# Performance work log

Measured on AMD Instinct MI355X. Metric: run time of the kernel, lower is better.

Reference implementation:

```python
import jax, jax.numpy as jnp
import numpy as np

NUM_USERS = 4096
NUM_ITEMS = 8192
EMBED_DIM = 64
NUM_LAYERS = 3


def setup_inputs() -> dict:
    key = jax.random.key(0)
    k1, k2 = jax.random.split(key)
    # embedding table for users+items (nn.Embedding init normal std=0.1)
    x = jax.random.normal(k1, (NUM_USERS + NUM_ITEMS, EMBED_DIM), dtype=jnp.float32) * 0.1
    # dense 0/1 user-item interaction matrix (forward applies torch.nonzero to it)
    edge_index = jax.random.randint(k2, (NUM_USERS, NUM_ITEMS), 0, 2, dtype=jnp.int32)
    return {"x": x, "edge_index": edge_index}


def reference(x, edge_index):
    U, I, L = NUM_USERS, NUM_ITEMS, NUM_LAYERS
    adj = edge_index.astype(jnp.float32)  # [U, I], 0/1
    # symmetric degree normalization: adj / sqrt(deg_u * deg_i), nan (0/0) -> 0
    deg_u = jnp.sum(adj, axis=1)  # [U]
    deg_i = jnp.sum(adj, axis=0)  # [I]
    denom = jnp.sqrt(deg_u[:, None] * deg_i[None, :])  # [U, I]
    weights = jnp.where(denom > 0, adj / jnp.where(denom > 0, denom, 1.0), 0.0)
    # weights is identical every layer (depends only on edge_index)
    acc = jnp.zeros_like(x)
    for _ in range(L):
        # NOTE: original code concatenates (item-side, user-side) in this order
        x = jnp.concatenate([weights.T @ x[:U], weights @ x[U:]], axis=0)  # [I+U, d]
        acc = acc + x
    # alpha = 1/(1+L) * ones applied to every layer output
    return acc / (1.0 + L)
```

## Files before the change

### kernel.cpp

```cpp
#include <hip/hip_runtime.h>

#define NU 4096
#define NI 8192
#define ND 64
#define NTOT 12288
#define CT 8
#define CB 16
#define BROW 520

typedef unsigned short u16;
typedef unsigned int u32;
typedef unsigned long long u64;

__device__ __forceinline__ u16 f2bf(float f) {
    union { float f; u32 u; } v; v.f = f;
    u32 u = v.u;
    u += 0x7FFFu + ((u >> 16) & 1u);
    return (u16)(u >> 16);
}

typedef short frag8 __attribute__((ext_vector_type(8)));
typedef float f32x4 __attribute__((ext_vector_type(4)));

__global__ __launch_bounds__(256) void k_pack2(const int* __restrict__ edge,
        u64* __restrict__ Apk, u64* __restrict__ ATpk) {
    __shared__ __align__(16) u16 At[256][40];
    __shared__ __align__(16) u64 Tt[512][6];
    const int t = threadIdx.x;
    const int u0 = (blockIdx.x >> 4) * 256;
    const int i0 = (blockIdx.x & 15) * 512;
    const int cg = t & 31;
    const int rb = t >> 5;

    #pragma unroll 4
    for (int rr = 0; rr < 32; rr++) {
        const int row = rb * 32 + rr;
        const int4* p = (const int4*)(edge + (size_t)(u0 + row) * NI + i0 + cg * 16);
        u32 bits = 0;
        #pragma unroll
        for (int m = 0; m < 4; m++) {
            int4 v = p[m];
            bits |= (v.x != 0 ? 1u : 0u) << (m * 4 + 0);
            bits |= (v.y != 0 ? 1u : 0u) << (m * 4 + 1);
            bits |= (v.z != 0 ? 1u : 0u) << (m * 4 + 2);
            bits |= (v.w != 0 ? 1u : 0u) << (m * 4 + 3);
        }
        At[row][cg] = (u16)bits;
    }
    __syncthreads();

    {
        u64* dst = Apk + (size_t)(u0 + t) * 128 + (i0 >> 6);
        #pragma unroll
        for (int q = 0; q < 4; q++) {
            uint4 v = *(const uint4*)&At[t][q * 8];
            *(uint4*)(dst + q * 2) = v;
        }
    }

    {
        const int lane = t & 63, w = t >> 6;
        const u64 M[6] = {0x00000000FFFFFFFFULL, 0x0000FFFF0000FFFFULL,
                          0x00FF00FF00FF00FFULL, 0x0F0F0F0F0F0F0F0FULL,
                          0x3333333333333333ULL, 0x5555555555555555ULL};
        #pragma unroll
        for (int sc = 0; sc < 8; sc++) {
            u64 x = *(const u64*)&At[w * 64 + lane][sc * 4];
            #pragma unroll
            for (int si = 0; si < 6; si++) {
                const int s = 32 >> si;
                u64 y = __shfl_xor(x, s, 64);
                x = (lane & s) ? ((x & ~M[si]) | ((y >> s) & M[si]))
                               : ((x &  M[si]) | ((y << s) & ~M[si]));
            }
            Tt[sc * 64 + lane][w] = x;
        }
    }
    __syncthreads();
    #pragma unroll
    for (int j = 0; j < 2; j++) {
        const int item = t * 2 + j;
        ulonglong2 a = *(const ulonglong2*)&Tt[item][0];
        ulonglong2 b = *(const ulonglong2*)&Tt[item][2];
        u64* dst = ATpk + (size_t)(i0 + item) * 64 + (u0 >> 6);
        *(ulonglong2*)dst = a;
        *(ulonglong2*)(dst + 2) = b;
    }
}

__global__ __launch_bounds__(256) void k_scale0(const float* __restrict__ x,
        const u64* __restrict__ Apk, const u64* __restrict__ ATpk,
        float* __restrict__ dsu, float* __restrict__ dsi,
        u16* __restrict__ BuT, u16* __restrict__ BiT) {
    __shared__ float sc[64];
    const int t = threadIdx.x;
    const int r0 = blockIdx.x * 64;
    {
        const int rl = t >> 2, part = t & 3;
        int cnt = 0;
        if (r0 < NU) {
            const u64* p = Apk + (size_t)(r0 + rl) * 128 + part * 32;
            #pragma unroll
            for (int i = 0; i < 32; i++) cnt += (int)__popcll(p[i]);
        } else {
            const u64* p = ATpk + (size_t)(r0 - NU + rl) * 64 + part * 16;
            #pragma unroll
            for (int i = 0; i < 16; i++) cnt += (int)__popcll(p[i]);
        }
        cnt += __shfl_xor(cnt, 1, 64);
        cnt += __shfl_xor(cnt, 2, 64);
        if (part == 0) {
            float s = cnt > 0 ? rsqrtf((float)cnt) : 0.f;
            sc[rl] = s;
            if (r0 < NU) dsu[r0 + rl] = s; else dsi[r0 - NU + rl] = s;
        }
    }
    __syncthreads();
    const int r4 = t >> 4, c4 = t & 15;
    float y[4][4];
    #pragma unroll
    for (int j = 0; j < 4; j++) {
        const int rl = r4 * 4 + j;
        const float s = sc[rl];
        float4 xv = *(const float4*)(x + (size_t)(r0 + rl) * ND + c4 * 4);
        y[j][0] = xv.x * s; y[j][1] = xv.y * s;
        y[j][2] = xv.z * s; y[j][3] = xv.w * s;
    }
    u16* dst; size_t stride; int col0;
    if (r0 < NU) { dst = BuT; stride = NU; col0 = r0; }
    else         { dst = BiT; stride = NI; col0 = r0 - NU; }
    #pragma unroll
    for (int k = 0; k < 4; k++) {
        ushort4 w;
        w.x = f2bf(y[0][k]); w.y = f2bf(y[1][k]);
        w.z = f2bf(y[2][k]); w.w = f2bf(y[3][k]);
        *(ushort4*)(dst + (size_t)(c4 * 4 + k) * stride + col0 + r4 * 4) = w;
    }
}

__global__ __launch_bounds__(256) void k_gemm(
        const u64* __restrict__ Apk, const u64* __restrict__ ATpk,
        const u16* __restrict__ BuT, const u16* __restrict__ BiT,
        float* __restrict__ Ptop, float* __restrict__ Pbot) {
    __shared__ __align__(16) u16 Bs[64 * BROW];
    const int t = threadIdx.x, bx = blockIdx.x;
    const int lane = t & 63, w = t >> 6, lr = lane & 15, lg = lane >> 4;
    const u64* arow; const u16* dense; int Kstr, wpr, kbase, pstr; float* Pout;
    if (bx < 1024) {
        const int tile = bx >> 3, chunk = bx & 7;
        arow = ATpk + (size_t)(tile * 64) * 64 + chunk * 8; wpr = 64;
        dense = BuT; Kstr = NU; kbase = chunk * 512; pstr = CT * 64;
        Pout = Ptop + (size_t)(tile * 64) * pstr + chunk * 64;
    } else {
        const int b2 = bx - 1024, tile = b2 >> 4, chunk = b2 & 15;
        arow = Apk + (size_t)(tile * 64) * 128 + chunk * 8; wpr = 128;
        dense = BiT; Kstr = NI; kbase = chunk * 512; pstr = CB * 64;
        Pout = Pbot + (size_t)(tile * 64) * pstr + chunk * 64;
    }
    const u16* gsrc = dense + kbase;
    #pragma unroll
    for (int it = 0; it < 16; it++) {
        const int e = it * 4 + w;
        __builtin_amdgcn_global_load_lds(
            (const __attribute__((address_space(1))) void*)
                (gsrc + (size_t)e * Kstr + lane * 8),
            (__attribute__((address_space(3))) void*)(&Bs[e * BROW]),
            16, 0, 0);
    }
    const u64* myrow = arow + (size_t)(w * 16 + lr) * wpr;
    u64 aw[8];
    #pragma unroll
    for (int qq = 0; qq < 4; qq++) {
        ulonglong2 v = *(const ulonglong2*)(myrow + qq * 2);
        aw[qq * 2] = v.x; aw[qq * 2 + 1] = v.y;
    }
    f32x4 acc[4];
    #pragma unroll
    for (int i = 0; i < 4; i++) acc[i] = f32x4{0.f, 0.f, 0.f, 0.f};
    __syncthreads();

    #pragma unroll
    for (int kk = 0; kk < 8; kk++) {
        const u32 lo = (u32)aw[kk], hi = (u32)(aw[kk] >> 32);
        const u32 byte0 = (lo >> (lg * 8)) & 0xFFu;
        const u32 byte1 = (hi >> (lg * 8)) & 0xFFu;
        frag8 bf0, bf1;
        #pragma unroll
        for (int j = 0; j < 8; j++) {
            bf0[j] = (short)(((byte0 >> j) & 1u) ? 0x3F80 : 0);
            bf1[j] = (short)(((byte1 >> j) & 1u) ? 0x3F80 : 0);
        }
        #pragma unroll
        for (int nt = 0; nt < 4; nt++) {
            const int e = nt * 16 + lr;
            frag8 a0 = *(const frag8*)&Bs[e * BROW + kk * 64 + lg * 8];
            frag8 a1 = *(const frag8*)&Bs[e * BROW + kk * 64 + 32 + lg * 8];
            acc[nt] = __builtin_amdgcn_mfma_f32_16x16x32_bf16(a0, bf0, acc[nt], 0, 0, 0);
            acc[nt] = __builtin_amdgcn_mfma_f32_16x16x32_bf16(a1, bf1, acc[nt], 0, 0, 0);
        }
    }
    __syncthreads();
    float* Fs = (float*)Bs;
    #pragma unroll
    for (int nt = 0; nt < 4; nt++) {
        const int row = w * 16 + lr, g = nt * 4 + lg;
        *(f32x4*)&Fs[row * 64 + (((g + row) & 15) * 4)] = acc[nt];
    }
    __syncthreads();
    #pragma unroll
    for (int ii = 0; ii < 4; ii++) {
        const int slot = t + ii * 256;
        const int row = slot >> 4, g = slot & 15;
        f32x4 v = *(const f32x4*)&Fs[row * 64 + (((g + row) & 15) * 4)];
        *(f32x4*)&Pout[(size_t)row * pstr + g * 4] = v;
    }
}

__global__ __launch_bounds__(256) void k_reduce(
        const float* __restrict__ Ptop, const float* __restrict__ Pbot,
        const float* __restrict__ dsu, const float* __restrict__ dsi,
        float* __restrict__ accbuf, u16* __restrict__ BuTn,
        u16* __restrict__ BiTn, float* __restrict__ out, int layer) {
    __shared__ u16 TB[64][24];
    const int t = threadIdx.x, bx = blockIdx.x;
    const int rl = t >> 4, e4 = t & 15;
    int grow; float so;
    float sx = 0.f, sy = 0.f, sz = 0.f, sw = 0.f;
    if (bx < 512) {
        grow = bx * 16 + rl;
        const float* p = Ptop + (size_t)grow * (CT * 64) + e4 * 4;
        #pragma unroll
        for (int c = 0; c < CT; c++) {
            float4 v = *(const float4*)(p + c * 64);
            sx += v.x; sy += v.y; sz += v.z; sw += v.w;
        }
        so = dsi[grow];
    } else {
        const int u = (bx - 512) * 16 + rl;
        grow = NI + u;
        const float* p = Pbot + (size_t)u * (CB * 64) + e4 * 4;
        #pragma unroll
        for (int c = 0; c < CB; c++) {
            float4 v = *(const float4*)(p + c * 64);
            sx += v.x; sy += v.y; sz += v.z; sw += v.w;
        }
        so = dsu[grow - NI];
    }
    float4 y;
    y.x = sx * so; y.y = sy * so; y.z = sz * so; y.w = sw * so;
    const size_t o = (size_t)grow * ND + e4 * 4;
    if (layer == 0) {
        *(float4*)(accbuf + o) = y;
    } else if (layer == 1) {
        float4 a = *(const float4*)(accbuf + o);
        a.x += y.x; a.y += y.y; a.z += y.z; a.w += y.w;
        *(float4*)(accbuf + o) = a;
    } else {
        float4 a = *(const float4*)(accbuf + o);
        a.x = (a.x + y.x) * 0.25f; a.y = (a.y + y.y) * 0.25f;
        a.z = (a.z + y.z) * 0.25f; a.w = (a.w + y.w) * 0.25f;
        *(float4*)(out + o) = a;
    }
    if (layer != 2) {
        const float fn = (grow < NU) ? dsu[grow] : dsi[grow - NU];
        TB[e4 * 4 + 0][rl] = f2bf(y.x * fn);
        TB[e4 * 4 + 1][rl] = f2bf(y.y * fn);
        TB[e4 * 4 + 2][rl] = f2bf(y.z * fn);
        TB[e4 * 4 + 3][rl] = f2bf(y.w * fn);
        __syncthreads();
        if (t < 128) {
            const int e = t >> 1, h = t & 1;
            u16* dst; size_t stride; int col0;
            if (bx < 256)      { dst = BuTn; stride = NU; col0 = bx * 16; }
            else if (bx < 512) { dst = BiTn; stride = NI; col0 = bx * 16 - NU; }
            else               { dst = BiTn; stride = NI; col0 = (bx - 512) * 16 + NI - NU; }
            uint4 v = *(const uint4*)&TB[e][h * 8];
            *(uint4*)(dst + (size_t)e * stride + col0 + h * 8) = v;
        }
    }
}

extern "C" void kernel_launch(void* const* d_in, const int* in_sizes, int n_in,
                              void* d_out, int out_size, void* d_ws, size_t ws_size,
                              hipStream_t stream) {
    (void)in_sizes; (void)n_in; (void)out_size; (void)ws_size;
    const float* x    = (const float*)d_in[0];
    const int*   edge = (const int*)d_in[1];
    float* out = (float*)d_out;

    char* ws = (char*)d_ws;
    size_t off = 0;
    u64* Apk  = (u64*)(ws + off); off += (size_t)NU * (NI / 64) * 8;
    u64* ATpk = (u64*)(ws + off); off += (size_t)NI * (NU / 64) * 8;
    float* dsu = (float*)(ws + off); off += (size_t)NU * 4;
    float* dsi = (float*)(ws + off); off += (size_t)NI * 4;
    u16* BuT0 = (u16*)(ws + off); off += (size_t)ND * NU * 2;
    u16* BuT1 = (u16*)(ws + off); off += (size_t)ND * NU * 2;
    u16* BiT0 = (u16*)(ws + off); off += (size_t)ND * NI * 2;
    u16* BiT1 = (u16*)(ws + off); off += (size_t)ND * NI * 2;
    float* acc  = (float*)(ws + off); off += (size_t)NTOT * ND * 4;
    float* Ptop = (float*)(ws + off); off += (size_t)NI * CT * 64 * 4;
    float* Pbot = (float*)(ws + off); off += (size_t)NU * CB * 64 * 4;

    k_pack2<<<256, 256, 0, stream>>>(edge, Apk, ATpk);
    k_scale0<<<NTOT / 64, 256, 0, stream>>>(x, Apk, ATpk, dsu, dsi, BuT0, BiT0);

    k_gemm<<<2048, 256, 0, stream>>>(Apk, ATpk, BuT0, BiT0, Ptop, Pbot);
    k_reduce<<<768, 256, 0, stream>>>(Ptop, Pbot, dsu, dsi, acc, BuT1, BiT1, out, 0);
    k_gemm<<<2048, 256, 0, stream>>>(Apk, ATpk, BuT1, BiT1, Ptop, Pbot);
    k_reduce<<<768, 256, 0, stream>>>(Ptop, Pbot, dsu, dsi, acc, BuT0, BiT0, out, 1);
    k_gemm<<<2048, 256, 0, stream>>>(Apk, ATpk, BuT0, BiT0, Ptop, Pbot);
    k_reduce<<<768, 256, 0, stream>>>(Ptop, Pbot, dsu, dsi, acc,
                                      (u16*)nullptr, (u16*)nullptr, out, 2);
}
```

Before: 287.9 us.

## Fuse split-K reduction into GEMM via last-block atomic counter; shrink pack tiles

```diff
diff --git a/kernel.cpp b/kernel.cpp
--- a/kernel.cpp
+++ b/kernel.cpp
@@ -7,6 +7,7 @@
 #define CT 8
 #define CB 16
 #define BROW 520
+#define NTILE 192
 
 typedef unsigned short u16;
 typedef unsigned int u32;
@@ -24,17 +25,17 @@
 
 __global__ __launch_bounds__(256) void k_pack2(const int* __restrict__ edge,
         u64* __restrict__ Apk, u64* __restrict__ ATpk) {
-    __shared__ __align__(16) u16 At[256][40];
-    __shared__ __align__(16) u64 Tt[512][6];
+    __shared__ __align__(16) u16 At[128][40];
+    __shared__ __align__(16) u64 Tt[512][2];
     const int t = threadIdx.x;
-    const int u0 = (blockIdx.x >> 4) * 256;
+    const int u0 = (blockIdx.x >> 4) * 128;
     const int i0 = (blockIdx.x & 15) * 512;
     const int cg = t & 31;
     const int rb = t >> 5;
 
     #pragma unroll 4
-    for (int rr = 0; rr < 32; rr++) {
-        const int row = rb * 32 + rr;
+    for (int rr = 0; rr < 16; rr++) {
+        const int row = rb * 16 + rr;
         const int4* p = (const int4*)(edge + (size_t)(u0 + row) * NI + i0 + cg * 16);
         u32 bits = 0;
         #pragma unroll
@@ -50,12 +51,12 @@
     __syncthreads();
 
     {
-        u64* dst = Apk + (size_t)(u0 + t) * 128 + (i0 >> 6);
-        #pragma unroll
-        for (int q = 0; q < 4; q++) {
-            uint4 v = *(const uint4*)&At[t][q * 8];
-            *(uint4*)(dst + q * 2) = v;
-        }
+        const int row = t >> 1, h = t & 1;
+        uint4 v0 = *(const uint4*)&At[row][h * 16];
+        uint4 v1 = *(const uint4*)&At[row][h * 16 + 8];
+        u64* dst = Apk + (size_t)(u0 + row) * 128 + (i0 >> 6) + h * 4;
+        *(uint4*)dst = v0;
+        *(uint4*)(dst + 2) = v1;
     }
 
     {
@@ -64,8 +65,10 @@
                           0x00FF00FF00FF00FFULL, 0x0F0F0F0F0F0F0F0FULL,
                           0x3333333333333333ULL, 0x5555555555555555ULL};
         #pragma unroll
-        for (int sc = 0; sc < 8; sc++) {
-            u64 x = *(const u64*)&At[w * 64 + lane][sc * 4];
+        for (int m = 0; m < 4; m++) {
+            const int id = m * 4 + w;
+            const int sr = id >> 3, sc = id & 7;
+            u64 x = *(const u64*)&At[sr * 64 + lane][sc * 4];
             #pragma unroll
             for (int si = 0; si < 6; si++) {
                 const int s = 32 >> si;
@@ -73,7 +76,7 @@
                 x = (lane & s) ? ((x & ~M[si]) | ((y >> s) & M[si]))
                                : ((x &  M[si]) | ((y << s) & ~M[si]));
             }
-            Tt[sc * 64 + lane][w] = x;
+            Tt[sc * 64 + lane][sr] = x;
         }
     }
     __syncthreads();
@@ -81,10 +84,7 @@
     for (int j = 0; j < 2; j++) {
         const int item = t * 2 + j;
         ulonglong2 a = *(const ulonglong2*)&Tt[item][0];
-        ulonglong2 b = *(const ulonglong2*)&Tt[item][2];
-        u64* dst = ATpk + (size_t)(i0 + item) * 64 + (u0 >> 6);
-        *(ulonglong2*)dst = a;
-        *(ulonglong2*)(dst + 2) = b;
+        *(ulonglong2*)(ATpk + (size_t)(i0 + item) * 64 + (u0 >> 6)) = a;
     }
 }
 
@@ -138,24 +138,32 @@
     }
 }
 
-__global__ __launch_bounds__(256) void k_gemm(
+__global__ __launch_bounds__(256) void k_gemmf(
         const u64* __restrict__ Apk, const u64* __restrict__ ATpk,
         const u16* __restrict__ BuT, const u16* __restrict__ BiT,
-        float* __restrict__ Ptop, float* __restrict__ Pbot) {
+        float* __restrict__ Ptop, float* __restrict__ Pbot,
+        const float* __restrict__ dsu, const float* __restrict__ dsi,
+        float* __restrict__ accbuf, u16* __restrict__ BuTn,
+        u16* __restrict__ BiTn, float* __restrict__ out,
+        int* __restrict__ cnt, int layer) {
     __shared__ __align__(16) u16 Bs[64 * BROW];
+    __shared__ int isLast;
     const int t = threadIdx.x, bx = blockIdx.x;
     const int lane = t & 63, w = t >> 6, lr = lane & 15, lg = lane >> 4;
-    const u64* arow; const u16* dense; int Kstr, wpr, kbase, pstr; float* Pout;
+    const u64* arow; const u16* dense; int Kstr, wpr, kbase, pstr, tile, tileId, nch;
+    float* Pout; bool top;
     if (bx < 1024) {
-        const int tile = bx >> 3, chunk = bx & 7;
+        tile = bx >> 3; const int chunk = bx & 7; top = true;
         arow = ATpk + (size_t)(tile * 64) * 64 + chunk * 8; wpr = 64;
         dense = BuT; Kstr = NU; kbase = chunk * 512; pstr = CT * 64;
         Pout = Ptop + (size_t)(tile * 64) * pstr + chunk * 64;
+        tileId = tile; nch = CT;
     } else {
-        const int b2 = bx - 1024, tile = b2 >> 4, chunk = b2 & 15;
+        const int b2 = bx - 1024; tile = b2 >> 4; const int chunk = b2 & 15; top = false;
         arow = Apk + (size_t)(tile * 64) * 128 + chunk * 8; wpr = 128;
         dense = BiT; Kstr = NI; kbase = chunk * 512; pstr = CB * 64;
         Pout = Pbot + (size_t)(tile * 64) * pstr + chunk * 64;
+        tileId = 128 + tile; nch = CB;
     }
     const u16* gsrc = dense + kbase;
     #pragma unroll
@@ -214,69 +222,86 @@
         f32x4 v = *(const f32x4*)&Fs[row * 64 + (((g + row) & 15) * 4)];
         *(f32x4*)&Pout[(size_t)row * pstr + g * 4] = v;
     }
-}
-
-__global__ __launch_bounds__(256) void k_reduce(
-        const float* __restrict__ Ptop, const float* __restrict__ Pbot,
-        const float* __restrict__ dsu, const float* __restrict__ dsi,
-        float* __restrict__ accbuf, u16* __restrict__ BuTn,
-        u16* __restrict__ BiTn, float* __restrict__ out, int layer) {
-    __shared__ u16 TB[64][24];
-    const int t = threadIdx.x, bx = blockIdx.x;
-    const int rl = t >> 4, e4 = t & 15;
+    __syncthreads();
+    if (t == 0) {
+        __builtin_amdgcn_fence(__ATOMIC_RELEASE, "agent");
+        int old = __hip_atomic_fetch_add(&cnt[tileId], 1,
+                                         __ATOMIC_RELAXED, __HIP_MEMORY_SCOPE_AGENT);
+        isLast = (old == nch - 1);
+    }
+    __syncthreads();
+    if (!isLast) return;
+
+    __builtin_amdgcn_fence(__ATOMIC_ACQUIRE, "agent");
+    const int r = t >> 2, q = t & 3;
     int grow; float so;
-    float sx = 0.f, sy = 0.f, sz = 0.f, sw = 0.f;
-    if (bx < 512) {
-        grow = bx * 16 + rl;
-        const float* p = Ptop + (size_t)grow * (CT * 64) + e4 * 4;
+    float4 s0 = {0,0,0,0}, s1 = {0,0,0,0}, s2 = {0,0,0,0}, s3 = {0,0,0,0};
+    if (top) {
+        grow = tile * 64 + r;
+        const float* p = Ptop + (size_t)grow * (CT * 64) + q * 16;
         #pragma unroll
         for (int c = 0; c < CT; c++) {
-            float4 v = *(const float4*)(p + c * 64);
-            sx += v.x; sy += v.y; sz += v.z; sw += v.w;
+            s0.x += p[c*64+0];  s0.y += p[c*64+1];  s0.z += p[c*64+2];  s0.w += p[c*64+3];
+            s1.x += p[c*64+4];  s1.y += p[c*64+5];  s1.z += p[c*64+6];  s1.w += p[c*64+7];
+            s2.x += p[c*64+8];  s2.y += p[c*64+9];  s2.z += p[c*64+10]; s2.w += p[c*64+11];
+            s3.x += p[c*64+12]; s3.y += p[c*64+13]; s3.z += p[c*64+14]; s3.w += p[c*64+15];
         }
         so = dsi[grow];
     } else {
-        const int u = (bx - 512) * 16 + rl;
+        const int u = tile * 64 + r;
         grow = NI + u;
-        const float* p = Pbot + (size_t)u * (CB * 64) + e4 * 4;
+        const float* p = Pbot + (size_t)u * (CB * 64) + q * 16;
         #pragma unroll
         for (int c = 0; c < CB; c++) {
-            float4 v = *(const float4*)(p + c * 64);
-            sx += v.x; sy += v.y; sz += v.z; sw += v.w;
-        }
-        so = dsu[grow - NI];
-    }
-    float4 y;
-    y.x = sx * so; y.y = sy * so; y.z = sz * so; y.w = sw * so;
-    const size_t o = (size_t)grow * ND + e4 * 4;
-    if (layer == 0) {
-        *(float4*)(accbuf + o) = y;
-    } else if (layer == 1) {
-        float4 a = *(const float4*)(accbuf + o);
-        a.x += y.x; a.y += y.y; a.z += y.z; a.w += y.w;
-        *(float4*)(accbuf + o) = a;
-    } else {
-        float4 a = *(const float4*)(accbuf + o);
-        a.x = (a.x + y.x) * 0.25f; a.y = (a.y + y.y) * 0.25f;
-        a.z = (a.z + y.z) * 0.25f; a.w = (a.w + y.w) * 0.25f;
-        *(float4*)(out + o) = a;
+            s0.x += p[c*64+0];  s0.y += p[c*64+1];  s0.z += p[c*64+2];  s0.w += p[c*64+3];
+            s1.x += p[c*64+4];  s1.y += p[c*64+5];  s1.z += p[c*64+6];  s1.w += p[c*64+7];
+            s2.x += p[c*64+8];  s2.y += p[c*64+9];  s2.z += p[c*64+10]; s2.w += p[c*64+11];
+            s3.x += p[c*64+12]; s3.y += p[c*64+13]; s3.z += p[c*64+14]; s3.w += p[c*64+15];
+        }
+        so = dsu[u];
+    }
+    float4 y[4];
+    y[0].x = s0.x*so; y[0].y = s0.y*so; y[0].z = s0.z*so; y[0].w = s0.w*so;
+    y[1].x = s1.x*so; y[1].y = s1.y*so; y[1].z = s1.z*so; y[1].w = s1.w*so;
+    y[2].x = s2.x*so; y[2].y = s2.y*so; y[2].z = s2.z*so; y[2].w = s2.w*so;
+    y[3].x = s3.x*so; y[3].y = s3.y*so; y[3].z = s3.z*so; y[3].w = s3.w*so;
+    #pragma unroll
+    for (int j = 0; j < 4; j++) {
+        const size_t o = (size_t)grow * ND + q * 16 + j * 4;
+        if (layer == 0) {
+            *(float4*)(accbuf + o) = y[j];
+        } else if (layer == 1) {
+            float4 a = *(const float4*)(accbuf + o);
+            a.x += y[j].x; a.y += y[j].y; a.z += y[j].z; a.w += y[j].w;
+            *(float4*)(accbuf + o) = a;
+        } else {
+            float4 a = *(const float4*)(accbuf + o);
+            a.x = (a.x + y[j].x) * 0.25f; a.y = (a.y + y[j].y) * 0.25f;
+            a.z = (a.z + y[j].z) * 0.25f; a.w = (a.w + y[j].w) * 0.25f;
+            *(float4*)(out + o) = a;
+        }
     }
     if (layer != 2) {
         const float fn = (grow < NU) ? dsu[grow] : dsi[grow - NU];
-        TB[e4 * 4 + 0][rl] = f2bf(y.x * fn);
-        TB[e4 * 4 + 1][rl] = f2bf(y.y * fn);
-        TB[e4 * 4 + 2][rl] = f2bf(y.z * fn);
-        TB[e4 * 4 + 3][rl] = f2bf(y.w * fn);
+        u16* TB = (u16*)Bs;
+        #pragma unroll
+        for (int j = 0; j < 4; j++) {
+            TB[(q * 16 + j * 4 + 0) * 72 + r] = f2bf(y[j].x * fn);
+            TB[(q * 16 + j * 4 + 1) * 72 + r] = f2bf(y[j].y * fn);
+            TB[(q * 16 + j * 4 + 2) * 72 + r] = f2bf(y[j].z * fn);
+            TB[(q * 16 + j * 4 + 3) * 72 + r] = f2bf(y[j].w * fn);
+        }
         __syncthreads();
-        if (t < 128) {
-            const int e = t >> 1, h = t & 1;
-            u16* dst; size_t stride; int col0;
-            if (bx < 256)      { dst = BuTn; stride = NU; col0 = bx * 16; }
-            else if (bx < 512) { dst = BiTn; stride = NI; col0 = bx * 16 - NU; }
-            else               { dst = BiTn; stride = NI; col0 = (bx - 512) * 16 + NI - NU; }
-            uint4 v = *(const uint4*)&TB[e][h * 8];
-            *(uint4*)(dst + (size_t)e * stride + col0 + h * 8) = v;
-        }
+        u16* dst; size_t stride; int col0;
+        if (top) {
+            if (tile < 64) { dst = BuTn; stride = NU; col0 = tile * 64; }
+            else           { dst = BiTn; stride = NI; col0 = tile * 64 - NU; }
+        } else             { dst = BiTn; stride = NI; col0 = (NI - NU) + tile * 64; }
+        const int n = t >> 2, part = t & 3;
+        uint4 a = *(const uint4*)&TB[n * 72 + part * 16];
+        uint4 b = *(const uint4*)&TB[n * 72 + part * 16 + 8];
+        *(uint4*)(dst + (size_t)n * stride + col0 + part * 16) = a;
+        *(uint4*)(dst + (size_t)n * stride + col0 + part * 16 + 8) = b;
     }
 }
 
@@ -301,15 +326,17 @@
     float* acc  = (float*)(ws + off); off += (size_t)NTOT * ND * 4;
     float* Ptop = (float*)(ws + off); off += (size_t)NI * CT * 64 * 4;
     float* Pbot = (float*)(ws + off); off += (size_t)NU * CB * 64 * 4;
-
-    k_pack2<<<256, 256, 0, stream>>>(edge, Apk, ATpk);
+    int* cnt = (int*)(ws + off); off += (size_t)3 * NTILE * 4;
+
+    hipMemsetAsync(cnt, 0, 3 * NTILE * sizeof(int), stream);
+    k_pack2<<<512, 256, 0, stream>>>(edge, Apk, ATpk);
     k_scale0<<<NTOT / 64, 256, 0, stream>>>(x, Apk, ATpk, dsu, dsi, BuT0, BiT0);
 
-    k_gemm<<<2048, 256, 0, stream>>>(Apk, ATpk, BuT0, BiT0, Ptop, Pbot);
-    k_reduce<<<768, 256, 0, stream>>>(Ptop, Pbot, dsu, dsi, acc, BuT1, BiT1, out, 0);
-    k_gemm<<<2048, 256, 0, stream>>>(Apk, ATpk, BuT1, BiT1, Ptop, Pbot);
-    k_reduce<<<768, 256, 0, stream>>>(Ptop, Pbot, dsu, dsi, acc, BuT0, BiT0, out, 1);
-    k_gemm<<<2048, 256, 0, stream>>>(Apk, ATpk, BuT0, BiT0, Ptop, Pbot);
-    k_reduce<<<768, 256, 0, stream>>>(Ptop, Pbot, dsu, dsi, acc,
-                                      (u16*)nullptr, (u16*)nullptr, out, 2);
-}
+    k_gemmf<<<2048, 256, 0, stream>>>(Apk, ATpk, BuT0, BiT0, Ptop, Pbot,
+                                      dsu, dsi, acc, BuT1, BiT1, out, cnt, 0);
+    k_gemmf<<<2048, 256, 0, stream>>>(Apk, ATpk, BuT1, BiT1, Ptop, Pbot,
+                                      dsu, dsi, acc, BuT0, BiT0, out, cnt + NTILE, 1);
+    k_gemmf<<<2048, 256, 0, stream>>>(Apk, ATpk, BuT0, BiT0, Ptop, Pbot,
+                                      dsu, dsi, acc, (u16*)nullptr, (u16*)nullptr,
+                                      out, cnt + 2 * NTILE, 2);
+}
```

After: 695.6 us. 142% more time.

## Load GEMM dense operand directly from global and halve pack tile height

Applied to the files above, without the earlier changes.

```diff
diff --git a/kernel.cpp b/kernel.cpp
--- a/kernel.cpp
+++ b/kernel.cpp
@@ -6,7 +6,6 @@
 #define NTOT 12288
 #define CT 8
 #define CB 16
-#define BROW 520
 
 typedef unsigned short u16;
 typedef unsigned int u32;
@@ -24,17 +23,17 @@
 
 __global__ __launch_bounds__(256) void k_pack2(const int* __restrict__ edge,
         u64* __restrict__ Apk, u64* __restrict__ ATpk) {
-    __shared__ __align__(16) u16 At[256][40];
-    __shared__ __align__(16) u64 Tt[512][6];
+    __shared__ __align__(16) u16 At[128][40];
+    __shared__ __align__(16) u64 Tt[512][2];
     const int t = threadIdx.x;
-    const int u0 = (blockIdx.x >> 4) * 256;
+    const int u0 = (blockIdx.x >> 4) * 128;
     const int i0 = (blockIdx.x & 15) * 512;
     const int cg = t & 31;
     const int rb = t >> 5;
 
     #pragma unroll 4
-    for (int rr = 0; rr < 32; rr++) {
-        const int row = rb * 32 + rr;
+    for (int rr = 0; rr < 16; rr++) {
+        const int row = rb * 16 + rr;
         const int4* p = (const int4*)(edge + (size_t)(u0 + row) * NI + i0 + cg * 16);
         u32 bits = 0;
         #pragma unroll
@@ -50,12 +49,12 @@
     __syncthreads();
 
     {
-        u64* dst = Apk + (size_t)(u0 + t) * 128 + (i0 >> 6);
-        #pragma unroll
-        for (int q = 0; q < 4; q++) {
-            uint4 v = *(const uint4*)&At[t][q * 8];
-            *(uint4*)(dst + q * 2) = v;
-        }
+        const int row = t >> 1, h = t & 1;
+        uint4 v0 = *(const uint4*)&At[row][h * 16];
+        uint4 v1 = *(const uint4*)&At[row][h * 16 + 8];
+        u64* dst = Apk + (size_t)(u0 + row) * 128 + (i0 >> 6) + h * 4;
+        *(uint4*)dst = v0;
+        *(uint4*)(dst + 2) = v1;
     }
 
     {
@@ -64,8 +63,10 @@
                           0x00FF00FF00FF00FFULL, 0x0F0F0F0F0F0F0F0FULL,
                           0x3333333333333333ULL, 0x5555555555555555ULL};
         #pragma unroll
-        for (int sc = 0; sc < 8; sc++) {
-            u64 x = *(const u64*)&At[w * 64 + lane][sc * 4];
+        for (int m = 0; m < 4; m++) {
+            const int id = m * 4 + w;
+            const int sr = id >> 3, sc = id & 7;
+            u64 x = *(const u64*)&At[sr * 64 + lane][sc * 4];
             #pragma unroll
             for (int si = 0; si < 6; si++) {
                 const int s = 32 >> si;
@@ -73,7 +74,7 @@
                 x = (lane & s) ? ((x & ~M[si]) | ((y >> s) & M[si]))
                                : ((x &  M[si]) | ((y << s) & ~M[si]));
             }
-            Tt[sc * 64 + lane][w] = x;
+            Tt[sc * 64 + lane][sr] = x;
         }
     }
     __syncthreads();
@@ -81,10 +82,7 @@
     for (int j = 0; j < 2; j++) {
         const int item = t * 2 + j;
         ulonglong2 a = *(const ulonglong2*)&Tt[item][0];
-        ulonglong2 b = *(const ulonglong2*)&Tt[item][2];
-        u64* dst = ATpk + (size_t)(i0 + item) * 64 + (u0 >> 6);
-        *(ulonglong2*)dst = a;
-        *(ulonglong2*)(dst + 2) = b;
+        *(ulonglong2*)(ATpk + (size_t)(i0 + item) * 64 + (u0 >> 6)) = a;
     }
 }
 
@@ -142,7 +140,7 @@
         const u64* __restrict__ Apk, const u64* __restrict__ ATpk,
         const u16* __restrict__ BuT, const u16* __restrict__ BiT,
         float* __restrict__ Ptop, float* __restrict__ Pbot) {
-    __shared__ __align__(16) u16 Bs[64 * BROW];
+    __shared__ __align__(16) float Fs[64 * 64];
     const int t = threadIdx.x, bx = blockIdx.x;
     const int lane = t & 63, w = t >> 6, lr = lane & 15, lg = lane >> 4;
     const u64* arow; const u16* dense; int Kstr, wpr, kbase, pstr; float* Pout;
@@ -157,16 +155,6 @@
         dense = BiT; Kstr = NI; kbase = chunk * 512; pstr = CB * 64;
         Pout = Pbot + (size_t)(tile * 64) * pstr + chunk * 64;
     }
-    const u16* gsrc = dense + kbase;
-    #pragma unroll
-    for (int it = 0; it < 16; it++) {
-        const int e = it * 4 + w;
-        __builtin_amdgcn_global_load_lds(
-            (const __attribute__((address_space(1))) void*)
-                (gsrc + (size_t)e * Kstr + lane * 8),
-            (__attribute__((address_space(3))) void*)(&Bs[e * BROW]),
-            16, 0, 0);
-    }
     const u64* myrow = arow + (size_t)(w * 16 + lr) * wpr;
     u64 aw[8];
     #pragma unroll
@@ -174,10 +162,14 @@
         ulonglong2 v = *(const ulonglong2*)(myrow + qq * 2);
         aw[qq * 2] = v.x; aw[qq * 2 + 1] = v.y;
     }
+    const u16* pb[4];
+    #pragma unroll
+    for (int nt = 0; nt < 4; nt++)
+        pb[nt] = dense + (size_t)(nt * 16 + lr) * Kstr + kbase + lg * 8;
+
     f32x4 acc[4];
     #pragma unroll
     for (int i = 0; i < 4; i++) acc[i] = f32x4{0.f, 0.f, 0.f, 0.f};
-    __syncthreads();
 
     #pragma unroll
     for (int kk = 0; kk < 8; kk++) {
@@ -192,15 +184,12 @@
         }
         #pragma unroll
         for (int nt = 0; nt < 4; nt++) {
-            const int e = nt * 16 + lr;
-            frag8 a0 = *(const frag8*)&Bs[e * BROW + kk * 64 + lg * 8];
-            frag8 a1 = *(const frag8*)&Bs[e * BROW + kk * 64 + 32 + lg * 8];
+            frag8 a0 = *(const frag8*)(pb[nt] + kk * 64);
+            frag8 a1 = *(const frag8*)(pb[nt] + kk * 64 + 32);
             acc[nt] = __builtin_amdgcn_mfma_f32_16x16x32_bf16(a0, bf0, acc[nt], 0, 0, 0);
             acc[nt] = __builtin_amdgcn_mfma_f32_16x16x32_bf16(a1, bf1, acc[nt], 0, 0, 0);
         }
     }
-    __syncthreads();
-    float* Fs = (float*)Bs;
     #pragma unroll
     for (int nt = 0; nt < 4; nt++) {
         const int row = w * 16 + lr, g = nt * 4 + lg;
@@ -302,7 +291,7 @@
     float* Ptop = (float*)(ws + off); off += (size_t)NI * CT * 64 * 4;
     float* Pbot = (float*)(ws + off); off += (size_t)NU * CB * 64 * 4;
 
-    k_pack2<<<256, 256, 0, stream>>>(edge, Apk, ATpk);
+    k_pack2<<<512, 256, 0, stream>>>(edge, Apk, ATpk);
     k_scale0<<<NTOT / 64, 256, 0, stream>>>(x, Apk, ATpk, dsu, dsi, BuT0, BiT0);
 
     k_gemm<<<2048, 256, 0, stream>>>(Apk, ATpk, BuT0, BiT0, Ptop, Pbot);
```

New measurement: 458.7 us. 1.59x slower.
